# Kernel optimization log

Measured on AMD Instinct MI355X. Metric: run time of the kernel, lower is better.

Reference implementation:

```python
import jax, jax.numpy as jnp
from jax import lax
import numpy as np

H, W = 2160, 3840
KSIZE = 31


def _gaussian_kernel(size: int) -> jnp.ndarray:
    # sigma per OpenCV convention used in the module
    sigma = 0.3 * ((size - 1) * 0.5 - 1) + 0.8
    d = jnp.arange(size, dtype=jnp.float32) - (size // 2)
    k1 = jnp.exp(-(d ** 2) / (2.0 * sigma ** 2))
    k1 = k1 / k1.sum()
    k2 = jnp.outer(k1, k1)  # [k, k]
    # depthwise kernel for groups=3: [out=3, in/groups=1, k, k]
    return jnp.broadcast_to(k2[None, None], (3, 1, size, size))


def setup_inputs() -> dict:
    key = jax.random.key(0)
    k_img, = jax.random.split(key, 1)
    image = jax.random.uniform(k_img, (1, 3, H, W), dtype=jnp.float32)  # already /255-normalized
    mask = jnp.zeros((1, 1, H, W), dtype=jnp.float32)
    # two blur regions (x, y, w, h) -> mask[:, :, y:y+h, x:x+w] = 1
    mask = mask.at[:, :, 400:1400, 600:2600].set(1.0)
    mask = mask.at[:, :, 100:500, 3000:3700].set(1.0)
    kernel = _gaussian_kernel(KSIZE)
    return {"image": image, "mask": mask, "kernel": kernel}


def reference(image, mask, kernel):
    # depthwise 2D Gaussian conv, SAME padding == padding=k//2 for odd k, stride 1
    blurred = lax.conv_general_dilated(
        image, kernel,
        window_strides=(1, 1), padding="SAME",
        feature_group_count=3,
        dimension_numbers=("NCHW", "OIHW", "NCHW"),
    )
    out = image * (1.0 - mask) + blurred * mask  # mask broadcasts over channel dim
    # squeeze batch, NCHW -> HWC, back to 0..255 scale (uint8 cast omitted for float baseline)
    return out[0].transpose(1, 2, 0) * 255.0
```

## Files before the change

### kernel.cpp

```cpp
#include <hip/hip_runtime.h>

#define HH 2160
#define WW 3840
#define K 31
#define RAD 15
#define TW 64
#define TH 16
#define IW 96
#define IH 46
#define NTHREADS 256
#define NF4 (IH * (IW / 4))
#define TMPW 100

#define GLDS(gp, lp) __builtin_amdgcn_global_load_lds(                         \
    (const __attribute__((address_space(1))) void*)(gp),                       \
    (__attribute__((address_space(3))) void*)(lp), 16, 0, 0)

__device__ __forceinline__ float fcomp(float4 v, int p) {
    switch (p) { case 0: return v.x; case 1: return v.y; case 2: return v.z; default: return v.w; }
}

__device__ __forceinline__ float uniformf(float x) {
    return __uint_as_float(__builtin_amdgcn_readfirstlane(__float_as_uint(x)));
}

__global__ __launch_bounds__(NTHREADS, 4) void blur_masked_kernel(
    const float* __restrict__ img, const float* __restrict__ mask,
    const float* __restrict__ kern, float* __restrict__ out)
{
    __shared__ float s_in[NF4 * 4];
    __shared__ float s_tmp[TH * TMPW];
    __shared__ float s_k1[K];

    const int b  = blockIdx.x;
    const int ty = b % 135;
    const int tx = b / 135;
    const int x0 = tx * TW;
    const int y0 = ty * TH;
    const int t  = threadIdx.x;

    const int hr  = t >> 4;
    const int hc0 = (t & 15) * 4;

    if (t < K) {
        float s = 0.f;
        const float* kr = kern + t * K;
        #pragma unroll
        for (int j = 0; j < K; ++j) s += kr[j];
        s_k1[t] = s;
    }

    const size_t HW = (size_t)HH * WW;
    const size_t pix0 = (size_t)(y0 + hr) * WW + (x0 + hc0);
    float4 mv = *(const float4*)(mask + pix0);
    float4 i0 = *(const float4*)(img + pix0);
    float4 i1 = *(const float4*)(img + HW + pix0);
    float4 i2 = *(const float4*)(img + 2 * HW + pix0);

    int anyLocal = (mv.x != 0.f) | (mv.y != 0.f) | (mv.z != 0.f) | (mv.w != 0.f);
    int any = __syncthreads_or(anyLocal);

    if (!any) {
        float* ob = out + pix0 * 3;
        *(float4*)(ob)     = make_float4(i0.x * 255.f, i1.x * 255.f, i2.x * 255.f, i0.y * 255.f);
        *(float4*)(ob + 4) = make_float4(i1.y * 255.f, i2.y * 255.f, i0.z * 255.f, i1.z * 255.f);
        *(float4*)(ob + 8) = make_float4(i2.z * 255.f, i0.w * 255.f, i1.w * 255.f, i2.w * 255.f);
        return;
    }

    float k1r[K];
    #pragma unroll
    for (int j = 0; j < K; ++j) k1r[j] = uniformf(s_k1[j]);

    const bool interior = (tx >= 1) && (tx <= 58) && (ty >= 1) && (ty <= 133);

    auto stage = [&](int ch) {
        const float* imc = img + (size_t)ch * HW;
        if (interior) {
            #pragma unroll
            for (int k2 = 0; k2 < 5; ++k2) {
                int i = t + k2 * NTHREADS;
                if (i < NF4) {
                    int r = i / (IW / 4), c4 = i % (IW / 4);
                    const float* gp = imc + (size_t)(y0 - RAD + r) * WW + (x0 - 16 + 4 * c4);
                    GLDS(gp, s_in + 4 * i);
                }
            }
        } else {
            #pragma unroll
            for (int k2 = 0; k2 < 5; ++k2) {
                int i = t + k2 * NTHREADS;
                if (i < NF4) {
                    int r = i / (IW / 4), c4 = i % (IW / 4);
                    int gy = y0 - RAD + r, gx = x0 - 16 + 4 * c4;
                    float4 v = make_float4(0.f, 0.f, 0.f, 0.f);
                    if (gy >= 0 && gy < HH && gx >= 0 && gx < WW)
                        v = *(const float4*)(imc + (size_t)gy * WW + gx);
                    *(float4*)(s_in + 4 * i) = v;
                }
            }
        }
    };

    stage(0);

    float o[12];

    const int vc = t % 96;
    const int vh = t / 96;

    #pragma unroll
    for (int ch = 0; ch < 3; ++ch) {
        __syncthreads();

        if (vh < 2) {
            float acc[8] = {0.f, 0.f, 0.f, 0.f, 0.f, 0.f, 0.f, 0.f};
            const int ybase = vh * 8;
            #pragma unroll
            for (int s = 0; s < 38; ++s) {
                float v = s_in[(ybase + s) * IW + vc];
                #pragma unroll
                for (int j = 0; j < 8; ++j) {
                    if (s - j >= 0 && s - j <= 30) acc[j] += v * k1r[s - j];
                }
            }
            #pragma unroll
            for (int j = 0; j < 8; ++j)
                s_tmp[(ybase + j) * TMPW + vc] = acc[j];
        }

        __syncthreads();

        if (ch < 2) stage(ch + 1);

        float a0 = 0.f, a1 = 0.f, a2 = 0.f, a3 = 0.f;
        const float* rowp = s_tmp + hr * TMPW + hc0;
        #pragma unroll
        for (int q = 0; q < 9; ++q) {
            float4 w = *(const float4*)(rowp + 4 * q);
            #pragma unroll
            for (int e = 0; e < 4; ++e) {
                const int idx = 4 * q + e;
                float v = fcomp(w, e);
                if (idx - 1 >= 0 && idx - 1 <= 30) a0 += v * k1r[idx - 1];
                if (idx - 2 >= 0 && idx - 2 <= 30) a1 += v * k1r[idx - 2];
                if (idx - 3 >= 0 && idx - 3 <= 30) a2 += v * k1r[idx - 3];
                if (idx - 4 >= 0 && idx - 4 <= 30) a3 += v * k1r[idx - 4];
            }
        }

        float4 iv = (ch == 0) ? i0 : (ch == 1) ? i1 : i2;
        float bl[4] = {a0, a1, a2, a3};
        #pragma unroll
        for (int p = 0; p < 4; ++p) {
            float m = fcomp(mv, p);
            o[p * 3 + ch] = (fcomp(iv, p) * (1.f - m) + bl[p] * m) * 255.f;
        }
    }

    float* ob = out + pix0 * 3;
    *(float4*)(ob)     = make_float4(o[0], o[1], o[2],  o[3]);
    *(float4*)(ob + 4) = make_float4(o[4], o[5], o[6],  o[7]);
    *(float4*)(ob + 8) = make_float4(o[8], o[9], o[10], o[11]);
}

extern "C" void kernel_launch(void* const* d_in, const int* in_sizes, int n_in,
                              void* d_out, int out_size, void* d_ws, size_t ws_size,
                              hipStream_t stream) {
    const float* img  = (const float*)d_in[0];
    const float* mask = (const float*)d_in[1];
    const float* kern = (const float*)d_in[2];
    float* out = (float*)d_out;
    int nblocks = 60 * 135;
    blur_masked_kernel<<<nblocks, NTHREADS, 0, stream>>>(img, mask, kern, out);
}
```

Measured before the change: 63.88 us.

## Double tile height, use packed vertical pass, read center pixels from LDS

```diff
diff --git a/kernel.cpp b/kernel.cpp
--- a/kernel.cpp
+++ b/kernel.cpp
@@ -5,12 +5,15 @@
 #define K 31
 #define RAD 15
 #define TW 64
-#define TH 16
+#define TH 32
 #define IW 96
-#define IH 46
+#define IH 62
 #define NTHREADS 256
 #define NF4 (IH * (IW / 4))
 #define TMPW 100
+#define NTY 68
+
+typedef float v2f __attribute__((ext_vector_type(2)));
 
 #define GLDS(gp, lp) __builtin_amdgcn_global_load_lds(                         \
     (const __attribute__((address_space(1))) void*)(gp),                       \
@@ -33,14 +36,17 @@
     __shared__ float s_k1[K];
 
     const int b  = blockIdx.x;
-    const int ty = b % 135;
-    const int tx = b / 135;
+    const int tx = b % 60;
+    const int ty = b / 60;
     const int x0 = tx * TW;
     const int y0 = ty * TH;
     const int t  = threadIdx.x;
 
     const int hr  = t >> 4;
     const int hc0 = (t & 15) * 4;
+    const int gyA = y0 + hr;
+    const int gyB = y0 + hr + 16;
+    const bool validB = (gyB < HH);
 
     if (t < K) {
         float s = 0.f;
@@ -51,20 +57,33 @@
     }
 
     const size_t HW = (size_t)HH * WW;
-    const size_t pix0 = (size_t)(y0 + hr) * WW + (x0 + hc0);
-    float4 mv = *(const float4*)(mask + pix0);
-    float4 i0 = *(const float4*)(img + pix0);
-    float4 i1 = *(const float4*)(img + HW + pix0);
-    float4 i2 = *(const float4*)(img + 2 * HW + pix0);
-
-    int anyLocal = (mv.x != 0.f) | (mv.y != 0.f) | (mv.z != 0.f) | (mv.w != 0.f);
+    const size_t pixA = (size_t)gyA * WW + (x0 + hc0);
+    const size_t pixB = (size_t)gyB * WW + (x0 + hc0);
+    float4 mvA = *(const float4*)(mask + pixA);
+    float4 mvB = make_float4(0.f, 0.f, 0.f, 0.f);
+    if (validB) mvB = *(const float4*)(mask + pixB);
+
+    int anyLocal = (mvA.x != 0.f) | (mvA.y != 0.f) | (mvA.z != 0.f) | (mvA.w != 0.f) |
+                   (mvB.x != 0.f) | (mvB.y != 0.f) | (mvB.z != 0.f) | (mvB.w != 0.f);
     int any = __syncthreads_or(anyLocal);
 
     if (!any) {
-        float* ob = out + pix0 * 3;
-        *(float4*)(ob)     = make_float4(i0.x * 255.f, i1.x * 255.f, i2.x * 255.f, i0.y * 255.f);
-        *(float4*)(ob + 4) = make_float4(i1.y * 255.f, i2.y * 255.f, i0.z * 255.f, i1.z * 255.f);
-        *(float4*)(ob + 8) = make_float4(i2.z * 255.f, i0.w * 255.f, i1.w * 255.f, i2.w * 255.f);
+        float4 a0 = *(const float4*)(img + pixA);
+        float4 a1 = *(const float4*)(img + HW + pixA);
+        float4 a2 = *(const float4*)(img + 2 * HW + pixA);
+        float* obA = out + pixA * 3;
+        *(float4*)(obA)     = make_float4(a0.x * 255.f, a1.x * 255.f, a2.x * 255.f, a0.y * 255.f);
+        *(float4*)(obA + 4) = make_float4(a1.y * 255.f, a2.y * 255.f, a0.z * 255.f, a1.z * 255.f);
+        *(float4*)(obA + 8) = make_float4(a2.z * 255.f, a0.w * 255.f, a1.w * 255.f, a2.w * 255.f);
+        if (validB) {
+            float4 b0 = *(const float4*)(img + pixB);
+            float4 b1 = *(const float4*)(img + HW + pixB);
+            float4 b2 = *(const float4*)(img + 2 * HW + pixB);
+            float* obB = out + pixB * 3;
+            *(float4*)(obB)     = make_float4(b0.x * 255.f, b1.x * 255.f, b2.x * 255.f, b0.y * 255.f);
+            *(float4*)(obB + 4) = make_float4(b1.y * 255.f, b2.y * 255.f, b0.z * 255.f, b1.z * 255.f);
+            *(float4*)(obB + 8) = make_float4(b2.z * 255.f, b0.w * 255.f, b1.w * 255.f, b2.w * 255.f);
+        }
         return;
     }
 
@@ -72,13 +91,13 @@
     #pragma unroll
     for (int j = 0; j < K; ++j) k1r[j] = uniformf(s_k1[j]);
 
-    const bool interior = (tx >= 1) && (tx <= 58) && (ty >= 1) && (ty <= 133);
+    const bool interior = (tx >= 1) && (tx <= 58) && (ty >= 1) && (ty <= 66);
 
     auto stage = [&](int ch) {
         const float* imc = img + (size_t)ch * HW;
         if (interior) {
             #pragma unroll
-            for (int k2 = 0; k2 < 5; ++k2) {
+            for (int k2 = 0; k2 < 6; ++k2) {
                 int i = t + k2 * NTHREADS;
                 if (i < NF4) {
                     int r = i / (IW / 4), c4 = i % (IW / 4);
@@ -88,7 +107,7 @@
             }
         } else {
             #pragma unroll
-            for (int k2 = 0; k2 < 5; ++k2) {
+            for (int k2 = 0; k2 < 6; ++k2) {
                 int i = t + k2 * NTHREADS;
                 if (i < NF4) {
                     int r = i / (IW / 4), c4 = i % (IW / 4);
@@ -104,64 +123,80 @@
 
     stage(0);
 
-    float o[12];
-
-    const int vc = t % 96;
-    const int vh = t / 96;
+    float oA[12], oB[12];
+
+    const int cp = t % 48;
+    const int vh = t / 48;
 
     #pragma unroll
     for (int ch = 0; ch < 3; ++ch) {
         __syncthreads();
 
-        if (vh < 2) {
-            float acc[8] = {0.f, 0.f, 0.f, 0.f, 0.f, 0.f, 0.f, 0.f};
+        if (vh < 4) {
+            v2f acc[8];
+            #pragma unroll
+            for (int a = 0; a < 8; ++a) acc[a] = 0.f;
             const int ybase = vh * 8;
             #pragma unroll
             for (int s = 0; s < 38; ++s) {
-                float v = s_in[(ybase + s) * IW + vc];
+                v2f v = *(const v2f*)&s_in[(ybase + s) * IW + 2 * cp];
                 #pragma unroll
-                for (int j = 0; j < 8; ++j) {
-                    if (s - j >= 0 && s - j <= 30) acc[j] += v * k1r[s - j];
+                for (int a = 0; a < 8; ++a) {
+                    if (s - a >= 0 && s - a <= 30) acc[a] += v * k1r[s - a];
                 }
             }
             #pragma unroll
-            for (int j = 0; j < 8; ++j)
-                s_tmp[(ybase + j) * TMPW + vc] = acc[j];
-        }
+            for (int a = 0; a < 8; ++a)
+                *(v2f*)&s_tmp[(ybase + a) * TMPW + 2 * cp] = acc[a];
+        }
+        float4 ivA = *(const float4*)(s_in + (hr + RAD) * IW + hc0 + 16);
+        float4 ivB = *(const float4*)(s_in + (hr + 16 + RAD) * IW + hc0 + 16);
 
         __syncthreads();
 
         if (ch < 2) stage(ch + 1);
 
-        float a0 = 0.f, a1 = 0.f, a2 = 0.f, a3 = 0.f;
-        const float* rowp = s_tmp + hr * TMPW + hc0;
+        float aA0 = 0.f, aA1 = 0.f, aA2 = 0.f, aA3 = 0.f;
+        float aB0 = 0.f, aB1 = 0.f, aB2 = 0.f, aB3 = 0.f;
+        const float* rowA = s_tmp + hr * TMPW + hc0;
+        const float* rowB = s_tmp + (hr + 16) * TMPW + hc0;
         #pragma unroll
         for (int q = 0; q < 9; ++q) {
-            float4 w = *(const float4*)(rowp + 4 * q);
+            float4 wA = *(const float4*)(rowA + 4 * q);
+            float4 wB = *(const float4*)(rowB + 4 * q);
             #pragma unroll
             for (int e = 0; e < 4; ++e) {
                 const int idx = 4 * q + e;
-                float v = fcomp(w, e);
-                if (idx - 1 >= 0 && idx - 1 <= 30) a0 += v * k1r[idx - 1];
-                if (idx - 2 >= 0 && idx - 2 <= 30) a1 += v * k1r[idx - 2];
-                if (idx - 3 >= 0 && idx - 3 <= 30) a2 += v * k1r[idx - 3];
-                if (idx - 4 >= 0 && idx - 4 <= 30) a3 += v * k1r[idx - 4];
-            }
-        }
-
-        float4 iv = (ch == 0) ? i0 : (ch == 1) ? i1 : i2;
-        float bl[4] = {a0, a1, a2, a3};
+                float vA = fcomp(wA, e);
+                float vB = fcomp(wB, e);
+                if (idx - 1 >= 0 && idx - 1 <= 30) { aA0 += vA * k1r[idx - 1]; aB0 += vB * k1r[idx - 1]; }
+                if (idx - 2 >= 0 && idx - 2 <= 30) { aA1 += vA * k1r[idx - 2]; aB1 += vB * k1r[idx - 2]; }
+                if (idx - 3 >= 0 && idx - 3 <= 30) { aA2 += vA * k1r[idx - 3]; aB2 += vB * k1r[idx - 3]; }
+                if (idx - 4 >= 0 && idx - 4 <= 30) { aA3 += vA * k1r[idx - 4]; aB3 += vB * k1r[idx - 4]; }
+            }
+        }
+
+        float blA[4] = {aA0, aA1, aA2, aA3};
+        float blB[4] = {aB0, aB1, aB2, aB3};
         #pragma unroll
         for (int p = 0; p < 4; ++p) {
-            float m = fcomp(mv, p);
-            o[p * 3 + ch] = (fcomp(iv, p) * (1.f - m) + bl[p] * m) * 255.f;
-        }
-    }
-
-    float* ob = out + pix0 * 3;
-    *(float4*)(ob)     = make_float4(o[0], o[1], o[2],  o[3]);
-    *(float4*)(ob + 4) = make_float4(o[4], o[5], o[6],  o[7]);
-    *(float4*)(ob + 8) = make_float4(o[8], o[9], o[10], o[11]);
+            float mA = fcomp(mvA, p);
+            float mB = fcomp(mvB, p);
+            oA[p * 3 + ch] = (fcomp(ivA, p) * (1.f - mA) + blA[p] * mA) * 255.f;
+            oB[p * 3 + ch] = (fcomp(ivB, p) * (1.f - mB) + blB[p] * mB) * 255.f;
+        }
+    }
+
+    float* obA = out + pixA * 3;
+    *(float4*)(obA)     = make_float4(oA[0], oA[1], oA[2],  oA[3]);
+    *(float4*)(obA + 4) = make_float4(oA[4], oA[5], oA[6],  oA[7]);
+    *(float4*)(obA + 8) = make_float4(oA[8], oA[9], oA[10], oA[11]);
+    if (validB) {
+        float* obB = out + pixB * 3;
+        *(float4*)(obB)     = make_float4(oB[0], oB[1], oB[2],  oB[3]);
+        *(float4*)(obB + 4) = make_float4(oB[4], oB[5], oB[6],  oB[7]);
+        *(float4*)(obB + 8) = make_float4(oB[8], oB[9], oB[10], oB[11]);
+    }
 }
 
 extern "C" void kernel_launch(void* const* d_in, const int* in_sizes, int n_in,
@@ -171,6 +206,6 @@
     const float* mask = (const float*)d_in[1];
     const float* kern = (const float*)d_in[2];
     float* out = (float*)d_out;
-    int nblocks = 60 * 135;
+    int nblocks = 60 * NTY;
     blur_masked_kernel<<<nblocks, NTHREADS, 0, stream>>>(img, mask, kern, out);
 }
```

Measured after the change: 94.59 us. +48.1%, slower.

## Reorder block mapping row-major and simplify halo staging address math

Applied to the files above, without the earlier changes.

```diff
diff --git a/kernel.cpp b/kernel.cpp
--- a/kernel.cpp
+++ b/kernel.cpp
@@ -9,7 +9,6 @@
 #define IW 96
 #define IH 46
 #define NTHREADS 256
-#define NF4 (IH * (IW / 4))
 #define TMPW 100
 
 #define GLDS(gp, lp) __builtin_amdgcn_global_load_lds(                         \
@@ -28,13 +27,13 @@
     const float* __restrict__ img, const float* __restrict__ mask,
     const float* __restrict__ kern, float* __restrict__ out)
 {
-    __shared__ float s_in[NF4 * 4];
+    __shared__ float s_in[IH * IW];
     __shared__ float s_tmp[TH * TMPW];
     __shared__ float s_k1[K];
 
     const int b  = blockIdx.x;
-    const int ty = b % 135;
-    const int tx = b / 135;
+    const int tx = b % 60;
+    const int ty = b / 60;
     const int x0 = tx * TW;
     const int y0 = ty * TH;
     const int t  = threadIdx.x;
@@ -74,29 +73,32 @@
 
     const bool interior = (tx >= 1) && (tx <= 58) && (ty >= 1) && (ty <= 133);
 
+    const int sr  = t / 24;
+    const int sc  = t % 24;
+    const bool sact = (t < 240);
+
     auto stage = [&](int ch) {
-        const float* imc = img + (size_t)ch * HW;
+        const float* gp0 = img + (size_t)ch * HW
+                         + (size_t)(y0 - RAD + sr) * WW + (x0 - 16 + 4 * sc);
+        float* lp0 = s_in + sr * IW + 4 * sc;
         if (interior) {
-            #pragma unroll
-            for (int k2 = 0; k2 < 5; ++k2) {
-                int i = t + k2 * NTHREADS;
-                if (i < NF4) {
-                    int r = i / (IW / 4), c4 = i % (IW / 4);
-                    const float* gp = imc + (size_t)(y0 - RAD + r) * WW + (x0 - 16 + 4 * c4);
-                    GLDS(gp, s_in + 4 * i);
+            if (sact) {
+                #pragma unroll
+                for (int k2 = 0; k2 < 5; ++k2) {
+                    if (sr + 10 * k2 < IH)
+                        GLDS(gp0 + (size_t)(10 * k2) * WW, lp0 + 10 * k2 * IW);
                 }
             }
         } else {
             #pragma unroll
             for (int k2 = 0; k2 < 5; ++k2) {
-                int i = t + k2 * NTHREADS;
-                if (i < NF4) {
-                    int r = i / (IW / 4), c4 = i % (IW / 4);
-                    int gy = y0 - RAD + r, gx = x0 - 16 + 4 * c4;
+                int r = sr + 10 * k2;
+                if (sact && r < IH) {
+                    int gy = y0 - RAD + r, gx = x0 - 16 + 4 * sc;
                     float4 v = make_float4(0.f, 0.f, 0.f, 0.f);
                     if (gy >= 0 && gy < HH && gx >= 0 && gx < WW)
-                        v = *(const float4*)(imc + (size_t)gy * WW + gx);
-                    *(float4*)(s_in + 4 * i) = v;
+                        v = *(const float4*)(img + (size_t)ch * HW + (size_t)gy * WW + gx);
+                    *(float4*)(s_in + r * IW + 4 * sc) = v;
                 }
             }
         }
```

After: 59.14 us. 7.4% less time.
